# Performance work log

Measured on AMD Instinct MI355X. Metric: run time of the kernel, lower is better.

The kernel has to match this reference:

```python
import jax, jax.numpy as jnp
import numpy as np

B, T, C, E = 8, 8192, 256, 64
CAPACITY_FACTOR = 1.25
TOP_K = 2


def setup_inputs() -> dict:
    key = jax.random.key(0)
    k1, k2, k3 = jax.random.split(key, 3)
    x = jax.random.normal(k1, (B, T, C), dtype=jnp.float32)
    W_gate = jax.random.normal(k2, (C, E), dtype=jnp.float32) / np.sqrt(C)
    W_experts = jax.random.normal(k3, (E, C, C), dtype=jnp.float32) / np.sqrt(C)
    return {"x": x, "W_gate": W_gate, "W_experts": W_experts}


def reference(x, W_gate, W_experts):
    b, t, c = x.shape
    e = W_gate.shape[1]
    n = b * t              # tokens
    s = n * TOP_K          # assignment slots, ordered (token i, slot j) like the torch loop
    capacity = max(1, int(CAPACITY_FACTOR * s / e))  # static python int

    logits = x @ W_gate                              # [B,T,E]
    gates = jax.nn.softmax(logits, axis=-1)
    scores, indices = jax.lax.top_k(gates, TOP_K)    # [B,T,2] (values are raw gate probs, no renorm)

    x_flat = x.reshape(n, c)
    eid = indices.reshape(s)                         # expert id per assignment, FIFO order i*2+j
    sc = scores.reshape(s)
    tok = jnp.repeat(jnp.arange(n), TOP_K)           # source token per assignment

    # FIFO rank of each assignment within its expert (matches the python capacity loop)
    onehot = jax.nn.one_hot(eid, e, dtype=jnp.int32)          # [S,E]
    rank = jnp.cumsum(onehot, axis=0)[jnp.arange(s), eid] - 1  # prior count of same expert
    keep = rank < capacity                                     # capacity-dropped tokens

    # Scatter tokens into per-expert buffers [E*capacity, C]; dropped slots go OOB -> 'drop'
    buf_idx = jnp.where(keep, eid * capacity + rank, e * capacity)
    buf = jnp.zeros((e * capacity, c), x.dtype).at[buf_idx].set(x_flat[tok], mode="drop")

    # Grouped GEMM: one Linear(C,C) per expert
    y = jnp.einsum("eck,ekd->ecd", buf.reshape(e, capacity, c), W_experts)
    y = y.reshape(e * capacity, c)

    # Gather back, scale by gate score, scatter-add into token positions
    safe_idx = jnp.where(keep, buf_idx, 0)
    contrib = jnp.where(keep[:, None], y[safe_idx] * sc[:, None], jnp.zeros((), x.dtype))
    combined = jnp.zeros((n, c), x.dtype).at[tok].add(contrib).reshape(b, t, c)

    load = gates.mean(axis=(0, 1))                  # [E]
    aux_loss = jnp.mean((load - 1.0 / e) ** 2)      # mse vs uniform
    return combined, aux_loss
```

## Files before the change

kernel.cpp:

```cpp
#include <hip/hip_runtime.h>
#include <stdint.h>

#define N_TOK   65536
#define S_SLOTS 131072
#define NEXP    64
#define CDIM    256
#define CAP     2560
#define NCHUNK  1024

typedef unsigned short u16;
typedef float    fvec4  __attribute__((ext_vector_type(4)));
typedef float    f32x4  __attribute__((ext_vector_type(4)));
typedef __bf16   bf16x8 __attribute__((ext_vector_type(8)));
typedef unsigned short u16x4 __attribute__((ext_vector_type(4)));

typedef __attribute__((address_space(1))) const void gvoid_t;
typedef __attribute__((address_space(3))) void       svoid_t;

__device__ __forceinline__ u16 f2bf(float f) {
  uint32_t u = __builtin_bit_cast(uint32_t, f);
  u += 0x7fffu + ((u >> 16) & 1u);
  return (u16)(u >> 16);
}
__device__ __forceinline__ float bf2f(u16 h) {
  return __builtin_bit_cast(float, (uint32_t)h << 16);
}
__device__ __forceinline__ void gload16(const void* g, void* l) {
  __builtin_amdgcn_global_load_lds(
      reinterpret_cast<gvoid_t*>(reinterpret_cast<uintptr_t>(g)),
      reinterpret_cast<svoid_t*>(reinterpret_cast<uintptr_t>(l)),
      16, 0, 0);
}

__global__ __launch_bounds__(256) void gating_kernel(
    const float* __restrict__ x, const float* __restrict__ Wg,
    u16* __restrict__ x_bf16, float* __restrict__ slot_score,
    int* __restrict__ slot_eid, float* __restrict__ load_g,
    int* __restrict__ chunk_hist)
{
  __shared__ float smem[8448];
  __shared__ int   hist_s[64];
  float* W_s   = smem;
  float* A_s   = smem + 4096;
  float* L_s   = smem;
  float* PMAXs = smem + 4160;
  float* PV1   = smem + 4416;
  int*   PI1   = (int*)(smem + 4672);
  float* PV2   = smem + 4928;
  int*   PI2   = (int*)(smem + 5184);
  float* PSUM  = smem + 5440;
  float* RINVs = smem + 5696;
  float* PLOAD = smem + 5760;

  const int t  = threadIdx.x;
  const int m0 = blockIdx.x * 64;
  const int ty = t >> 4, tx = t & 15;

  if (t < 64) hist_s[t] = 0;

  float acc[4][4];
#pragma unroll
  for (int j = 0; j < 4; ++j)
#pragma unroll
    for (int i = 0; i < 4; ++i) acc[j][i] = 0.f;

  for (int kt = 0; kt < 4; ++kt) {
    const int k0 = kt * 64;
#pragma unroll
    for (int p = 0; p < 4; ++p) {
      int idx = p * 1024 + t * 4;
      int kk = idx >> 6, e = idx & 63;
      *(fvec4*)&W_s[kk * 64 + e] = *(const fvec4*)&Wg[(size_t)(k0 + kk) * 64 + e];
    }
#pragma unroll
    for (int p = 0; p < 4; ++p) {
      int idx = p * 1024 + t * 4;
      int m = idx >> 6, k = idx & 63;
      fvec4 v = *(const fvec4*)&x[(size_t)(m0 + m) * 256 + k0 + k];
      *(fvec4*)&A_s[m * 68 + k] = v;
      u16x4 h;
      h.x = f2bf(v.x); h.y = f2bf(v.y); h.z = f2bf(v.z); h.w = f2bf(v.w);
      *(u16x4*)&x_bf16[(size_t)(m0 + m) * 256 + k0 + k] = h;
    }
    __syncthreads();
#pragma unroll
    for (int k4 = 0; k4 < 16; ++k4) {
      fvec4 av[4], bv[4];
#pragma unroll
      for (int j = 0; j < 4; ++j)
        av[j] = *(const fvec4*)&A_s[(ty * 4 + j) * 68 + k4 * 4];
#pragma unroll
      for (int kk = 0; kk < 4; ++kk)
        bv[kk] = *(const fvec4*)&W_s[(k4 * 4 + kk) * 64 + tx * 4];
#pragma unroll
      for (int j = 0; j < 4; ++j)
#pragma unroll
        for (int i = 0; i < 4; ++i) {
          acc[j][i] = fmaf(av[j][0], bv[0][i], acc[j][i]);
          acc[j][i] = fmaf(av[j][1], bv[1][i], acc[j][i]);
          acc[j][i] = fmaf(av[j][2], bv[2][i], acc[j][i]);
          acc[j][i] = fmaf(av[j][3], bv[3][i], acc[j][i]);
        }
    }
    __syncthreads();
  }

#pragma unroll
  for (int j = 0; j < 4; ++j)
#pragma unroll
    for (int i = 0; i < 4; ++i)
      L_s[(ty * 4 + j) * 65 + tx * 4 + i] = acc[j][i];
  __syncthreads();

  const int w = t >> 6, lane = t & 63;

  float pm = -3.4e38f, a1 = -3.4e38f, a2 = -3.4e38f;
  int   j1 = 0, j2 = 0;
#pragma unroll
  for (int ii = 0; ii < 16; ++ii) {
    int e = w * 16 + ii;
    float lg = L_s[lane * 65 + e];
    pm = fmaxf(pm, lg);
    if (lg > a1)      { a2 = a1; j2 = j1; a1 = lg; j1 = e; }
    else if (lg > a2) { a2 = lg; j2 = e; }
  }
  PMAXs[w * 64 + lane] = pm;
  PV1[w * 64 + lane] = a1; PI1[w * 64 + lane] = j1;
  PV2[w * 64 + lane] = a2; PI2[w * 64 + lane] = j2;
  __syncthreads();

  float m  = PMAXs[lane];
  float v1 = PV1[lane]; int i1 = PI1[lane];
  float v2 = PV2[lane]; int i2 = PI2[lane];
#pragma unroll
  for (int ww = 1; ww < 4; ++ww) {
    m = fmaxf(m, PMAXs[ww * 64 + lane]);
    float b1 = PV1[ww * 64 + lane]; int bi1 = PI1[ww * 64 + lane];
    float b2 = PV2[ww * 64 + lane]; int bi2 = PI2[ww * 64 + lane];
    if (b1 > v1) {
      if (v1 >= b2) { v2 = v1; i2 = i1; } else { v2 = b2; i2 = bi2; }
      v1 = b1; i1 = bi1;
    } else if (b1 > v2) { v2 = b1; i2 = bi1; }
  }

  float s = 0.f;
#pragma unroll
  for (int ii = 0; ii < 16; ++ii) {
    int e = w * 16 + ii;
    float E = __expf(L_s[lane * 65 + e] - m);
    L_s[lane * 65 + e] = E;
    s += E;
  }
  PSUM[w * 64 + lane] = s;
  __syncthreads();

  if (w == 0) {
    float rs = PSUM[lane] + PSUM[64 + lane] + PSUM[128 + lane] + PSUM[192 + lane];
    float ri = 1.0f / rs;
    RINVs[lane] = ri;
    float sc1 = L_s[lane * 65 + i1] * ri;
    float sc2 = L_s[lane * 65 + i2] * ri;
    int tg = m0 + lane;
    slot_eid[2 * tg]     = i1;
    slot_eid[2 * tg + 1] = i2;
    slot_score[2 * tg]     = sc1;
    slot_score[2 * tg + 1] = sc2;
    atomicAdd(&hist_s[i1], 1);
    atomicAdd(&hist_s[i2], 1);
  }
  __syncthreads();

  {
    float sl = 0.f;
#pragma unroll
    for (int jj = 0; jj < 16; ++jj) {
      int j = w * 16 + jj;
      sl = fmaf(L_s[j * 65 + lane], RINVs[j], sl);
    }
    PLOAD[t] = sl;
  }
  __syncthreads();
  if (t < 64) {
    float sl = PLOAD[t] + PLOAD[64 + t] + PLOAD[128 + t] + PLOAD[192 + t];
    atomicAdd(&load_g[t], sl);
    chunk_hist[blockIdx.x * 64 + t] = hist_s[t];
  }
}

__global__ __launch_bounds__(256) void wtrans_kernel(
    const float* __restrict__ W, u16* __restrict__ WT)
{
  __shared__ float tile[64 * 65];
  const int b = blockIdx.x;
  const int e = b >> 4, tt = b & 15;
  const int k0 = (tt >> 2) * 64, d0 = (tt & 3) * 64;
  const int t = threadIdx.x;
  const int j = t & 63, i0 = t >> 6;
  const float* We = W + (size_t)e * 65536;
#pragma unroll
  for (int p = 0; p < 16; ++p) {
    int i = p * 4 + i0;
    tile[i * 65 + j] = We[(size_t)(k0 + i) * 256 + d0 + j];
  }
  __syncthreads();
  u16* WTe = WT + (size_t)e * 65536;
#pragma unroll
  for (int p = 0; p < 16; ++p) {
    int d = p * 4 + i0;
    WTe[(size_t)(d0 + d) * 256 + k0 + j] = f2bf(tile[j * 65 + d]);
  }
}

__global__ __launch_bounds__(256) void scan_kernel(int* __restrict__ hist)
{
  const int e = blockIdx.x;
  const int t = threadIdx.x;
  const int lane = t & 63, w = t >> 6;
  int h[4];
#pragma unroll
  for (int i = 0; i < 4; ++i) h[i] = hist[(t * 4 + i) * 64 + e];
  int local = h[0] + h[1] + h[2] + h[3];
  int v = local;
#pragma unroll
  for (int off = 1; off < 64; off <<= 1) {
    int u = __shfl_up(v, off);
    if (lane >= off) v += u;
  }
  __shared__ int wtot[4];
  if (lane == 63) wtot[w] = v;
  __syncthreads();
  int woff = 0;
  for (int i = 0; i < w; ++i) woff += wtot[i];
  int excl = woff + v - local;
  hist[(t * 4 + 0) * 64 + e] = excl;
  hist[(t * 4 + 1) * 64 + e] = excl + h[0];
  hist[(t * 4 + 2) * 64 + e] = excl + h[0] + h[1];
  hist[(t * 4 + 3) * 64 + e] = excl + h[0] + h[1] + h[2];
}

__global__ __launch_bounds__(128) void rank_kernel(
    const int* __restrict__ slot_eid, const int* __restrict__ base,
    int* __restrict__ slot2buf, int* __restrict__ row_token)
{
  const int c = blockIdx.x;
  const int t = threadIdx.x;
  const int s = c * 128 + t;
  const int lane = t & 63, w = t >> 6;
  const int e = slot_eid[s];
  __shared__ int hist0[64];
  if (t < 64) hist0[t] = 0;
  __syncthreads();
  int rank = 0, cnt = 0;
#pragma unroll
  for (int k = 0; k < 64; ++k) {
    int eo = __shfl(e, k);
    bool m = (eo == e);
    rank += (m && k < lane) ? 1 : 0;
    cnt  += m ? 1 : 0;
  }
  if (w == 0 && rank == cnt - 1) hist0[e] = cnt;
  __syncthreads();
  int g = base[c * 64 + e] + rank + (w ? hist0[e] : 0);
  if (g < CAP) {
    slot2buf[s] = e * CAP + g;
    row_token[e * CAP + g] = s >> 1;
  } else {
    slot2buf[s] = -1;
  }
}

__global__ __launch_bounds__(256) void gemm_kernel(
    const u16* __restrict__ x_bf16, const u16* __restrict__ WT,
    const int* __restrict__ row_token, u16* __restrict__ y)
{
  __shared__ u16 A_s[128 * 32];
  __shared__ u16 B_s[128 * 32];
  __shared__ int tok_s[128];

  const int b = blockIdx.x;
  const int e = b / 40;
  const int r = b % 40;
  const int m0 = (r >> 1) * 128, n0 = (r & 1) * 128;
  const int t = threadIdx.x;

  if (t < 128) tok_s[t] = row_token[e * CAP + m0 + t];
  __syncthreads();

  const int w = t >> 6, lane = t & 63;
  const int rsub = lane >> 2;
  const int koff = (lane & 3) * 8;

  const int ra0 = w * 32 + rsub;
  const int ra1 = ra0 + 16;
  const char* pa0 = (const char*)(x_bf16 + (size_t)tok_s[ra0] * 256 + koff);
  const char* pa1 = (const char*)(x_bf16 + (size_t)tok_s[ra1] * 256 + koff);
  const u16* WTe = WT + (size_t)e * 65536;
  const char* pb0 = (const char*)(WTe + (size_t)(n0 + ra0) * 256 + koff);
  const char* pb1 = (const char*)(WTe + (size_t)(n0 + ra1) * 256 + koff);

  char* ldsA0 = (char*)A_s + (w * 32) * 64;
  char* ldsA1 = (char*)A_s + (w * 32 + 16) * 64;
  char* ldsB0 = (char*)B_s + (w * 32) * 64;
  char* ldsB1 = (char*)B_s + (w * 32 + 16) * 64;

  const int wm = w & 1, wn = w >> 1;
  const int lr = lane & 15, q = lane >> 4;

  f32x4 acc[4][4];
#pragma unroll
  for (int mt = 0; mt < 4; ++mt)
#pragma unroll
    for (int nt = 0; nt < 4; ++nt) acc[mt][nt] = (f32x4){0.f, 0.f, 0.f, 0.f};

  for (int kt = 0; kt < 8; ++kt) {
    gload16(pa0, ldsA0);
    gload16(pa1, ldsA1);
    gload16(pb0, ldsB0);
    gload16(pb1, ldsB1);
    __syncthreads();
    bf16x8 af[4], bg[4];
#pragma unroll
    for (int mt = 0; mt < 4; ++mt)
      af[mt] = *(const bf16x8*)&A_s[(wm * 64 + mt * 16 + lr) * 32 + q * 8];
#pragma unroll
    for (int nt = 0; nt < 4; ++nt)
      bg[nt] = *(const bf16x8*)&B_s[(wn * 64 + nt * 16 + lr) * 32 + q * 8];
#pragma unroll
    for (int mt = 0; mt < 4; ++mt)
#pragma unroll
      for (int nt = 0; nt < 4; ++nt)
        acc[mt][nt] = __builtin_amdgcn_mfma_f32_16x16x32_bf16(
            af[mt], bg[nt], acc[mt][nt], 0, 0, 0);
    __syncthreads();
    pa0 += 64; pa1 += 64; pb0 += 64; pb1 += 64;
  }

  u16* ye = y + (size_t)e * CAP * 256;
#pragma unroll
  for (int mt = 0; mt < 4; ++mt) {
    int grow = m0 + wm * 64 + mt * 16 + q * 4;
#pragma unroll
    for (int nt = 0; nt < 4; ++nt) {
      int gcol = n0 + wn * 64 + nt * 16 + lr;
#pragma unroll
      for (int rr = 0; rr < 4; ++rr)
        ye[(size_t)(grow + rr) * 256 + gcol] = f2bf(acc[mt][nt][rr]);
    }
  }
}

__global__ __launch_bounds__(256) void combine_kernel(
    const u16* __restrict__ y, const int* __restrict__ slot2buf,
    const float* __restrict__ slot_score, float* __restrict__ out)
{
  const int tok  = blockIdx.x * 4 + (threadIdx.x >> 6);
  const int lane = threadIdx.x & 63;
  const int   p0 = slot2buf[2 * tok],   p1 = slot2buf[2 * tok + 1];
  const float s0 = slot_score[2 * tok], s1 = slot_score[2 * tok + 1];
  float o0 = 0.f, o1 = 0.f, o2 = 0.f, o3 = 0.f;
  if (p0 >= 0) {
    u16x4 h = *(const u16x4*)&y[(size_t)p0 * 256 + lane * 4];
    o0 = fmaf(s0, bf2f(h.x), o0); o1 = fmaf(s0, bf2f(h.y), o1);
    o2 = fmaf(s0, bf2f(h.z), o2); o3 = fmaf(s0, bf2f(h.w), o3);
  }
  if (p1 >= 0) {
    u16x4 h = *(const u16x4*)&y[(size_t)p1 * 256 + lane * 4];
    o0 = fmaf(s1, bf2f(h.x), o0); o1 = fmaf(s1, bf2f(h.y), o1);
    o2 = fmaf(s1, bf2f(h.z), o2); o3 = fmaf(s1, bf2f(h.w), o3);
  }
  fvec4 o = {o0, o1, o2, o3};
  *(fvec4*)&out[(size_t)tok * 256 + lane * 4] = o;
}

__global__ __launch_bounds__(64) void aux_kernel(
    const float* __restrict__ load_g, float* __restrict__ out_aux)
{
  const int lane = threadIdx.x;
  float l = load_g[lane] * (1.0f / 65536.0f) - (1.0f / 64.0f);
  float v = l * l;
#pragma unroll
  for (int off = 1; off < 64; off <<= 1) v += __shfl_xor(v, off);
  if (lane == 0) out_aux[0] = v * (1.0f / 64.0f);
}

extern "C" void kernel_launch(void* const* d_in, const int* in_sizes, int n_in,
                              void* d_out, int out_size, void* d_ws, size_t ws_size,
                              hipStream_t stream)
{
  const float* x  = (const float*)d_in[0];
  const float* Wg = (const float*)d_in[1];
  const float* We = (const float*)d_in[2];
  float* out = (float*)d_out;

  char* ws = (char*)d_ws;
  float* slot_score = (float*)(ws + 0);
  int*   slot_eid   = (int*)(ws + 524288);
  int*   slot2buf   = (int*)(ws + 1048576);
  int*   row_token  = (int*)(ws + 1572864);
  float* load_g     = (float*)(ws + 2228224);
  int*   chunk_hist = (int*)(ws + 2359296);
  u16*   x_bf16     = (u16*)(ws + 4194304);
  u16*   WT         = (u16*)(ws + 37748736);
  u16*   y          = (u16*)(ws + 46137344);

  hipMemsetAsync(row_token, 0, 655360, stream);
  hipMemsetAsync(load_g, 0, 256, stream);

  gating_kernel<<<1024, 256, 0, stream>>>(x, Wg, x_bf16, slot_score, slot_eid,
                                          load_g, chunk_hist);
  wtrans_kernel<<<1024, 256, 0, stream>>>(We, WT);
  scan_kernel<<<64, 256, 0, stream>>>(chunk_hist);
  rank_kernel<<<1024, 128, 0, stream>>>(slot_eid, chunk_hist, slot2buf, row_token);
  gemm_kernel<<<2560, 256, 0, stream>>>(x_bf16, WT, row_token, y);
  combine_kernel<<<16384, 256, 0, stream>>>(y, slot2buf, slot_score, out);
  aux_kernel<<<1, 64, 0, stream>>>(load_g, out + 16777216);
}
```

Before: 239.1 us.

## Restructure gating kernel to one wave with register softmax and async LDS loads

The gating kernel now runs as a single 64-thread wave per 64-token block, with each thread computing an 8x8 logit tile. It double-buffers x and W_gate through LDS using direct global-to-LDS loads with an XOR swizzle, then does top-2, softmax and load accumulation in registers with wave shuffles instead of LDS round trips and block barriers. The bf16 conversion of x moves to a separate pass after the GEMM that rereads x, likely from cache. The aim is fewer barriers and less shared-memory traffic, but each block has a quarter of the threads, so latency hiding across the 1024 blocks is reduced.

Measured after the change: 436.6 us. 1.83x slower.

```diff
diff --git a/kernel.cpp b/kernel.cpp
--- a/kernel.cpp
+++ b/kernel.cpp
@@ -32,159 +32,152 @@
       16, 0, 0);
 }
 
-__global__ __launch_bounds__(256) void gating_kernel(
+__global__ __launch_bounds__(64) void gating_kernel(
     const float* __restrict__ x, const float* __restrict__ Wg,
     u16* __restrict__ x_bf16, float* __restrict__ slot_score,
     int* __restrict__ slot_eid, float* __restrict__ load_g,
     int* __restrict__ chunk_hist)
 {
-  __shared__ float smem[8448];
+  __shared__ float A_s[2][64 * 32];
+  __shared__ float W_s[2][32 * 64];
   __shared__ int   hist_s[64];
-  float* W_s   = smem;
-  float* A_s   = smem + 4096;
-  float* L_s   = smem;
-  float* PMAXs = smem + 4160;
-  float* PV1   = smem + 4416;
-  int*   PI1   = (int*)(smem + 4672);
-  float* PV2   = smem + 4928;
-  int*   PI2   = (int*)(smem + 5184);
-  float* PSUM  = smem + 5440;
-  float* RINVs = smem + 5696;
-  float* PLOAD = smem + 5760;
 
   const int t  = threadIdx.x;
   const int m0 = blockIdx.x * 64;
-  const int ty = t >> 4, tx = t & 15;
-
-  if (t < 64) hist_s[t] = 0;
-
-  float acc[4][4];
-#pragma unroll
-  for (int j = 0; j < 4; ++j)
-#pragma unroll
-    for (int i = 0; i < 4; ++i) acc[j][i] = 0.f;
-
-  for (int kt = 0; kt < 4; ++kt) {
-    const int k0 = kt * 64;
-#pragma unroll
-    for (int p = 0; p < 4; ++p) {
-      int idx = p * 1024 + t * 4;
-      int kk = idx >> 6, e = idx & 63;
-      *(fvec4*)&W_s[kk * 64 + e] = *(const fvec4*)&Wg[(size_t)(k0 + kk) * 64 + e];
-    }
-#pragma unroll
-    for (int p = 0; p < 4; ++p) {
-      int idx = p * 1024 + t * 4;
-      int m = idx >> 6, k = idx & 63;
-      fvec4 v = *(const fvec4*)&x[(size_t)(m0 + m) * 256 + k0 + k];
-      *(fvec4*)&A_s[m * 68 + k] = v;
+  const int ty = t >> 3, tx = t & 7;
+
+  hist_s[t] = 0;
+
+  float acc[8][8];
+#pragma unroll
+  for (int j = 0; j < 8; ++j)
+#pragma unroll
+    for (int i = 0; i < 8; ++i) acc[j][i] = 0.f;
+
+#define STAGE(B, K0)                                                          \
+  {                                                                           \
+    _Pragma("unroll")                                                         \
+    for (int p = 0; p < 8; ++p)                                               \
+      gload16(&x[(size_t)(m0 + p * 8 + ty) * 256 + (K0) + ((tx ^ p) << 2)],   \
+              &A_s[B][p * 256]);                                              \
+    _Pragma("unroll")                                                         \
+    for (int p = 0; p < 8; ++p)                                               \
+      gload16(&Wg[(size_t)((K0) + p * 4 + (t >> 4)) * 64 + (t & 15) * 4],     \
+              &W_s[B][p * 256]);                                              \
+  }
+
+  STAGE(0, 0);
+  __syncthreads();
+
+  int buf = 0;
+  for (int kt = 0; kt < 8; ++kt) {
+    if (kt < 7) {
+      if (buf == 0) STAGE(1, (kt + 1) * 32) else STAGE(0, (kt + 1) * 32);
+    }
+    const float* Ab = A_s[buf];
+    const float* Wb = W_s[buf];
+#pragma unroll
+    for (int k4 = 0; k4 < 8; ++k4) {
+      fvec4 av[8];
+#pragma unroll
+      for (int j = 0; j < 8; ++j)
+        av[j] = *(const fvec4*)&Ab[(ty * 8 + j) * 32 + ((k4 ^ ty) << 2)];
+#pragma unroll
+      for (int kk = 0; kk < 4; ++kk) {
+        fvec4 b0 = *(const fvec4*)&Wb[(k4 * 4 + kk) * 64 + tx * 8];
+        fvec4 b1 = *(const fvec4*)&Wb[(k4 * 4 + kk) * 64 + tx * 8 + 4];
+#pragma unroll
+        for (int j = 0; j < 8; ++j) {
+          float a = av[j][kk];
+          acc[j][0] = fmaf(a, b0.x, acc[j][0]);
+          acc[j][1] = fmaf(a, b0.y, acc[j][1]);
+          acc[j][2] = fmaf(a, b0.z, acc[j][2]);
+          acc[j][3] = fmaf(a, b0.w, acc[j][3]);
+          acc[j][4] = fmaf(a, b1.x, acc[j][4]);
+          acc[j][5] = fmaf(a, b1.y, acc[j][5]);
+          acc[j][6] = fmaf(a, b1.z, acc[j][6]);
+          acc[j][7] = fmaf(a, b1.w, acc[j][7]);
+        }
+      }
+    }
+    __syncthreads();
+    buf ^= 1;
+  }
+#undef STAGE
+
+  {
+    const float* xb = x + (size_t)m0 * 256;
+    u16* xh = x_bf16 + (size_t)m0 * 256;
+#pragma unroll 8
+    for (int p = 0; p < 64; ++p) {
+      fvec4 v = *(const fvec4*)&xb[(p * 64 + t) * 4];
       u16x4 h;
       h.x = f2bf(v.x); h.y = f2bf(v.y); h.z = f2bf(v.z); h.w = f2bf(v.w);
-      *(u16x4*)&x_bf16[(size_t)(m0 + m) * 256 + k0 + k] = h;
-    }
-    __syncthreads();
-#pragma unroll
-    for (int k4 = 0; k4 < 16; ++k4) {
-      fvec4 av[4], bv[4];
-#pragma unroll
-      for (int j = 0; j < 4; ++j)
-        av[j] = *(const fvec4*)&A_s[(ty * 4 + j) * 68 + k4 * 4];
-#pragma unroll
-      for (int kk = 0; kk < 4; ++kk)
-        bv[kk] = *(const fvec4*)&W_s[(k4 * 4 + kk) * 64 + tx * 4];
-#pragma unroll
-      for (int j = 0; j < 4; ++j)
-#pragma unroll
-        for (int i = 0; i < 4; ++i) {
-          acc[j][i] = fmaf(av[j][0], bv[0][i], acc[j][i]);
-          acc[j][i] = fmaf(av[j][1], bv[1][i], acc[j][i]);
-          acc[j][i] = fmaf(av[j][2], bv[2][i], acc[j][i]);
-          acc[j][i] = fmaf(av[j][3], bv[3][i], acc[j][i]);
-        }
-    }
-    __syncthreads();
-  }
-
-#pragma unroll
-  for (int j = 0; j < 4; ++j)
-#pragma unroll
-    for (int i = 0; i < 4; ++i)
-      L_s[(ty * 4 + j) * 65 + tx * 4 + i] = acc[j][i];
-  __syncthreads();
-
-  const int w = t >> 6, lane = t & 63;
-
-  float pm = -3.4e38f, a1 = -3.4e38f, a2 = -3.4e38f;
-  int   j1 = 0, j2 = 0;
-#pragma unroll
-  for (int ii = 0; ii < 16; ++ii) {
-    int e = w * 16 + ii;
-    float lg = L_s[lane * 65 + e];
-    pm = fmaxf(pm, lg);
-    if (lg > a1)      { a2 = a1; j2 = j1; a1 = lg; j1 = e; }
-    else if (lg > a2) { a2 = lg; j2 = e; }
-  }
-  PMAXs[w * 64 + lane] = pm;
-  PV1[w * 64 + lane] = a1; PI1[w * 64 + lane] = j1;
-  PV2[w * 64 + lane] = a2; PI2[w * 64 + lane] = j2;
-  __syncthreads();
-
-  float m  = PMAXs[lane];
-  float v1 = PV1[lane]; int i1 = PI1[lane];
-  float v2 = PV2[lane]; int i2 = PI2[lane];
-#pragma unroll
-  for (int ww = 1; ww < 4; ++ww) {
-    m = fmaxf(m, PMAXs[ww * 64 + lane]);
-    float b1 = PV1[ww * 64 + lane]; int bi1 = PI1[ww * 64 + lane];
-    float b2 = PV2[ww * 64 + lane]; int bi2 = PI2[ww * 64 + lane];
-    if (b1 > v1) {
-      if (v1 >= b2) { v2 = v1; i2 = i1; } else { v2 = b2; i2 = bi2; }
-      v1 = b1; i1 = bi1;
-    } else if (b1 > v2) { v2 = b1; i2 = bi1; }
-  }
-
-  float s = 0.f;
-#pragma unroll
-  for (int ii = 0; ii < 16; ++ii) {
-    int e = w * 16 + ii;
-    float E = __expf(L_s[lane * 65 + e] - m);
-    L_s[lane * 65 + e] = E;
-    s += E;
-  }
-  PSUM[w * 64 + lane] = s;
-  __syncthreads();
-
-  if (w == 0) {
-    float rs = PSUM[lane] + PSUM[64 + lane] + PSUM[128 + lane] + PSUM[192 + lane];
-    float ri = 1.0f / rs;
-    RINVs[lane] = ri;
-    float sc1 = L_s[lane * 65 + i1] * ri;
-    float sc2 = L_s[lane * 65 + i2] * ri;
-    int tg = m0 + lane;
-    slot_eid[2 * tg]     = i1;
-    slot_eid[2 * tg + 1] = i2;
-    slot_score[2 * tg]     = sc1;
-    slot_score[2 * tg + 1] = sc2;
-    atomicAdd(&hist_s[i1], 1);
-    atomicAdd(&hist_s[i2], 1);
-  }
-  __syncthreads();
-
-  {
-    float sl = 0.f;
-#pragma unroll
-    for (int jj = 0; jj < 16; ++jj) {
-      int j = w * 16 + jj;
-      sl = fmaf(L_s[j * 65 + lane], RINVs[j], sl);
-    }
-    PLOAD[t] = sl;
-  }
-  __syncthreads();
-  if (t < 64) {
-    float sl = PLOAD[t] + PLOAD[64 + t] + PLOAD[128 + t] + PLOAD[192 + t];
-    atomicAdd(&load_g[t], sl);
-    chunk_hist[blockIdx.x * 64 + t] = hist_s[t];
-  }
+      *(u16x4*)&xh[(p * 64 + t) * 4] = h;
+    }
+  }
+
+  const int e0 = tx * 8;
+  float pl[8];
+#pragma unroll
+  for (int i = 0; i < 8; ++i) pl[i] = 0.f;
+
+#pragma unroll
+  for (int j = 0; j < 8; ++j) {
+    float v1 = -3.4e38f, v2 = -3.4e38f; int i1 = 0, i2 = 0;
+#pragma unroll
+    for (int i = 0; i < 8; ++i) {
+      float lg = acc[j][i];
+      if (lg > v1)      { v2 = v1; i2 = i1; v1 = lg; i1 = e0 + i; }
+      else if (lg > v2) { v2 = lg; i2 = e0 + i; }
+    }
+#pragma unroll
+    for (int off = 1; off < 8; off <<= 1) {
+      float b1 = __shfl_xor(v1, off); int bi1 = __shfl_xor(i1, off);
+      float b2 = __shfl_xor(v2, off); int bi2 = __shfl_xor(i2, off);
+      bool w1 = (b1 > v1) || (b1 == v1 && bi1 < i1);
+      if (w1) {
+        bool k2 = (v1 > b2) || (v1 == b2 && i1 < bi2);
+        v2 = k2 ? v1 : b2; i2 = k2 ? i1 : bi2;
+        v1 = b1; i1 = bi1;
+      } else {
+        bool k2 = (b1 > v2) || (b1 == v2 && bi1 < i2);
+        if (k2) { v2 = b1; i2 = bi1; }
+      }
+    }
+    float m = v1;
+    float ex[8]; float s = 0.f;
+#pragma unroll
+    for (int i = 0; i < 8; ++i) { ex[i] = __expf(acc[j][i] - m); s += ex[i]; }
+#pragma unroll
+    for (int off = 1; off < 8; off <<= 1) s += __shfl_xor(s, off);
+    float ri = 1.0f / s;
+#pragma unroll
+    for (int i = 0; i < 8; ++i) pl[i] = fmaf(ex[i], ri, pl[i]);
+
+    if (tx == 0) {
+      int tok = m0 + ty * 8 + j;
+      slot_eid[2 * tok]     = i1;
+      slot_eid[2 * tok + 1] = i2;
+      slot_score[2 * tok]     = __expf(v1 - m) * ri;
+      slot_score[2 * tok + 1] = __expf(v2 - m) * ri;
+      atomicAdd(&hist_s[i1], 1);
+      atomicAdd(&hist_s[i2], 1);
+    }
+  }
+
+#pragma unroll
+  for (int i = 0; i < 8; ++i) {
+#pragma unroll
+    for (int off = 8; off < 64; off <<= 1) pl[i] += __shfl_xor(pl[i], off);
+  }
+  if (t < 8) {
+#pragma unroll
+    for (int i = 0; i < 8; ++i) atomicAdd(&load_g[t * 8 + i], pl[i]);
+  }
+
+  __syncthreads();
+  chunk_hist[blockIdx.x * 64 + t] = hist_s[t];
 }
 
 __global__ __launch_bounds__(256) void wtrans_kernel(
@@ -406,8 +399,8 @@
   hipMemsetAsync(row_token, 0, 655360, stream);
   hipMemsetAsync(load_g, 0, 256, stream);
 
-  gating_kernel<<<1024, 256, 0, stream>>>(x, Wg, x_bf16, slot_score, slot_eid,
-                                          load_g, chunk_hist);
+  gating_kernel<<<1024, 64, 0, stream>>>(x, Wg, x_bf16, slot_score, slot_eid,
+                                         load_g, chunk_hist);
   wtrans_kernel<<<1024, 256, 0, stream>>>(We, WT);
   scan_kernel<<<64, 256, 0, stream>>>(chunk_hist);
   rank_kernel<<<1024, 128, 0, stream>>>(slot_eid, chunk_hist, slot2buf, row_token);
```

## Double GEMM K-tile to 64 and XOR-swizzle LDS layout

Applied to the files above, without the earlier changes.

The expert GEMM now stages a 64-wide K slice per iteration instead of 32, which halves the number of K iterations and the barriers they need. The LDS tiles use an XOR swizzle on 16-byte chunks, applied on both the global-to-LDS load and the fragment reads, to avoid bank conflicts. This doubles LDS use per block, which may reduce occupancy, and the global loads are now issued as four 8-row groups per wave.

After: 235.8 us. Within noise of the previous version (-1.4%).

```diff
diff --git a/kernel.cpp b/kernel.cpp
--- a/kernel.cpp
+++ b/kernel.cpp
@@ -273,8 +273,8 @@
     const u16* __restrict__ x_bf16, const u16* __restrict__ WT,
     const int* __restrict__ row_token, u16* __restrict__ y)
 {
-  __shared__ u16 A_s[128 * 32];
-  __shared__ u16 B_s[128 * 32];
+  __shared__ u16 A_s[128 * 64];
+  __shared__ u16 B_s[128 * 64];
   __shared__ int tok_s[128];
 
   const int b = blockIdx.x;
@@ -287,21 +287,11 @@
   __syncthreads();
 
   const int w = t >> 6, lane = t & 63;
-  const int rsub = lane >> 2;
-  const int koff = (lane & 3) * 8;
-
-  const int ra0 = w * 32 + rsub;
-  const int ra1 = ra0 + 16;
-  const char* pa0 = (const char*)(x_bf16 + (size_t)tok_s[ra0] * 256 + koff);
-  const char* pa1 = (const char*)(x_bf16 + (size_t)tok_s[ra1] * 256 + koff);
+  const int rsub8 = lane >> 3;
+  const int c8    = lane & 7;
+  const int csw   = (c8 ^ rsub8) * 8;
+
   const u16* WTe = WT + (size_t)e * 65536;
-  const char* pb0 = (const char*)(WTe + (size_t)(n0 + ra0) * 256 + koff);
-  const char* pb1 = (const char*)(WTe + (size_t)(n0 + ra1) * 256 + koff);
-
-  char* ldsA0 = (char*)A_s + (w * 32) * 64;
-  char* ldsA1 = (char*)A_s + (w * 32 + 16) * 64;
-  char* ldsB0 = (char*)B_s + (w * 32) * 64;
-  char* ldsB1 = (char*)B_s + (w * 32 + 16) * 64;
 
   const int wm = w & 1, wn = w >> 1;
   const int lr = lane & 15, q = lane >> 4;
@@ -312,27 +302,38 @@
 #pragma unroll
     for (int nt = 0; nt < 4; ++nt) acc[mt][nt] = (f32x4){0.f, 0.f, 0.f, 0.f};
 
-  for (int kt = 0; kt < 8; ++kt) {
-    gload16(pa0, ldsA0);
-    gload16(pa1, ldsA1);
-    gload16(pb0, ldsB0);
-    gload16(pb1, ldsB1);
+  for (int kt = 0; kt < 4; ++kt) {
+    const int k0 = kt * 64;
+#pragma unroll
+    for (int i = 0; i < 4; ++i) {
+      int ra = w * 32 + i * 8 + rsub8;
+      gload16(x_bf16 + (size_t)tok_s[ra] * 256 + k0 + csw,
+              (char*)A_s + (size_t)(w * 32 + i * 8) * 128);
+      gload16(WTe + (size_t)(n0 + ra) * 256 + k0 + csw,
+              (char*)B_s + (size_t)(w * 32 + i * 8) * 128);
+    }
     __syncthreads();
-    bf16x8 af[4], bg[4];
-#pragma unroll
-    for (int mt = 0; mt < 4; ++mt)
-      af[mt] = *(const bf16x8*)&A_s[(wm * 64 + mt * 16 + lr) * 32 + q * 8];
-#pragma unroll
-    for (int nt = 0; nt < 4; ++nt)
-      bg[nt] = *(const bf16x8*)&B_s[(wn * 64 + nt * 16 + lr) * 32 + q * 8];
-#pragma unroll
-    for (int mt = 0; mt < 4; ++mt)
-#pragma unroll
-      for (int nt = 0; nt < 4; ++nt)
-        acc[mt][nt] = __builtin_amdgcn_mfma_f32_16x16x32_bf16(
-            af[mt], bg[nt], acc[mt][nt], 0, 0, 0);
+#pragma unroll
+    for (int kk = 0; kk < 2; ++kk) {
+      bf16x8 af[4], bg[4];
+#pragma unroll
+      for (int mt = 0; mt < 4; ++mt) {
+        int row = wm * 64 + mt * 16 + lr;
+        af[mt] = *(const bf16x8*)&A_s[row * 64 + (((kk * 4 + q) ^ (lr & 7)) * 8)];
+      }
+#pragma unroll
+      for (int nt = 0; nt < 4; ++nt) {
+        int row = wn * 64 + nt * 16 + lr;
+        bg[nt] = *(const bf16x8*)&B_s[row * 64 + (((kk * 4 + q) ^ (lr & 7)) * 8)];
+      }
+#pragma unroll
+      for (int mt = 0; mt < 4; ++mt)
+#pragma unroll
+        for (int nt = 0; nt < 4; ++nt)
+          acc[mt][nt] = __builtin_amdgcn_mfma_f32_16x16x32_bf16(
+              af[mt], bg[nt], acc[mt][nt], 0, 0, 0);
+    }
     __syncthreads();
-    pa0 += 64; pa1 += 64; pb0 += 64; pb1 += 64;
   }
 
   u16* ye = y + (size_t)e * CAP * 256;
```
